# Kernel tuning notes

Hardware: AMD Instinct MI355X
Metric: run time of the kernel (lower is better)

Reference implementation:

```python
import jax, jax.numpy as jnp
import numpy as np

DIM = 256
HEADS = 8
HEAD_DIM = DIM // HEADS
B_, N = 8192, 49


def setup_inputs() -> dict:
    key = jax.random.key(0)
    k1, k2, k3, k4, k5, k6 = jax.random.split(key, 6)
    x = jax.random.normal(k1, (B_, N, DIM), dtype=jnp.float32)
    mask = jax.random.normal(k2, (B_, N, N), dtype=jnp.float32)
    s = 1.0 / np.sqrt(DIM)
    W_qkv = jax.random.normal(k3, (3 * DIM, DIM), dtype=jnp.float32) * s
    b_qkv = jax.random.normal(k4, (3 * DIM,), dtype=jnp.float32) * 0.02
    W_proj = jax.random.normal(k5, (DIM, DIM), dtype=jnp.float32) * s
    b_proj = jax.random.normal(k6, (DIM,), dtype=jnp.float32) * 0.02
    return {"x": x, "mask": mask, "W_qkv": W_qkv, "b_qkv": b_qkv,
            "W_proj": W_proj, "b_proj": b_proj}


def reference(x, mask, W_qkv, b_qkv, W_proj, b_proj):
    B, n, C = x.shape
    scale = HEAD_DIM ** (-0.5)
    # qkv projection: (B, N, 3C) -> (3, B, H, N, hd)
    qkv = x @ W_qkv.T + b_qkv
    qkv = qkv.reshape(B, n, 3, HEADS, HEAD_DIM).transpose(2, 0, 3, 1, 4)
    q, k, v = qkv[0], qkv[1], qkv[2]
    # scaled dot-product within each window
    attn = jnp.einsum('bhqd,bhkd->bhqk', q, k) * scale
    attn = attn + mask[:, None, :, :]  # additive window mask
    attn = jax.nn.softmax(attn, axis=-1)
    out = jnp.einsum('bhqk,bhkd->bhqd', attn, v)
    out = out.transpose(0, 2, 1, 3).reshape(B, n, C)
    return out @ W_proj.T + b_proj
```

## Files before the change

kernel.cpp:

```cpp
#include <hip/hip_runtime.h>
#include <hip/hip_bf16.h>

#define NTOK 49
#define DIMC 256

typedef __attribute__((ext_vector_type(8))) short bf16x8;
typedef __attribute__((ext_vector_type(4))) float f32x4;

__device__ __forceinline__ unsigned f2bf(float f) {
    union { float f; unsigned u; } v; v.f = f;
    return (v.u + 0x7FFFu + ((v.u >> 16) & 1u)) >> 16;
}

__global__ void convert_weights(const float* __restrict__ wq, const float* __restrict__ wp,
                                unsigned short* __restrict__ wqb, unsigned short* __restrict__ wpb) {
    int i = blockIdx.x * 256 + threadIdx.x;
    if (i < 768 * 256) wqb[i] = (unsigned short)f2bf(wq[i]);
    if (i < 256 * 256) wpb[i] = (unsigned short)f2bf(wp[i]);
}

__launch_bounds__(512, 2)
__global__ void win_attn_fused(const float* __restrict__ x, const float* __restrict__ mask,
                               const unsigned short* __restrict__ wqb, const float* __restrict__ bqkv,
                               const unsigned short* __restrict__ wpb, const float* __restrict__ bproj,
                               float* __restrict__ out) {
    __shared__ __align__(16) char lds[147456];
    char* const xb  = lds;
    char* const qb  = lds + 32768;
    char* const kb  = lds + 65536;
    char* const vtb = lds + 98304;
    char* const mb  = lds + 131072;

    const int b = blockIdx.x;
    const int tid = threadIdx.x;
    const int lane = tid & 63;
    const int wid = tid >> 6;
    const int c = lane & 15;
    const int g = lane >> 4;

    const f32x4 fzero = {0.f, 0.f, 0.f, 0.f};

    {
        const float* xw = x + (size_t)b * (NTOK * DIMC);
        #pragma unroll
        for (int it = 0; it < 8; ++it) {
            int idx = it * 512 + tid;
            int t = idx >> 6;
            int d0 = (idx & 63) * 4;
            float4 v = make_float4(0.f, 0.f, 0.f, 0.f);
            if (t < NTOK) v = *(const float4*)(xw + t * DIMC + d0);
            unsigned lo = f2bf(v.x) | (f2bf(v.y) << 16);
            unsigned hi = f2bf(v.z) | (f2bf(v.w) << 16);
            *(uint2*)(xb + t * 512 + ((d0 * 2) ^ ((t & 7) << 4))) = make_uint2(lo, hi);
        }
        const float* mw = mask + (size_t)b * (NTOK * NTOK);
        #pragma unroll
        for (int it = 0; it < 8; ++it) {
            int idx = it * 512 + tid;
            int q = idx >> 6;
            int key = idx & 63;
            float v;
            if (q < NTOK && key < NTOK) v = mw[q * NTOK + key];
            else v = (key >= NTOK) ? -1e30f : 0.f;
            *(float*)(mb + q * 256 + ((key * 4) ^ ((q & 7) << 4))) = v;
        }
    }
    __syncthreads();

    {
        f32x4 acc[6][4];
        #pragma unroll
        for (int j = 0; j < 6; ++j)
            #pragma unroll
            for (int mt = 0; mt < 4; ++mt)
                acc[j][mt] = fzero;

        #pragma unroll
        for (int ks = 0; ks < 8; ++ks) {
            const int kk = ks * 32 + g * 8;
            bf16x8 af[4];
            #pragma unroll
            for (int mt = 0; mt < 4; ++mt) {
                int t = mt * 16 + c;
                af[mt] = *(const bf16x8*)(xb + t * 512 + ((kk * 2) ^ ((t & 7) << 4)));
            }
            #pragma unroll
            for (int j = 0; j < 6; ++j) {
                int o = (wid + 8 * j) * 16 + c;
                bf16x8 bfr = *(const bf16x8*)(wqb + (size_t)o * 256 + kk);
                #pragma unroll
                for (int mt = 0; mt < 4; ++mt)
                    acc[j][mt] = __builtin_amdgcn_mfma_f32_16x16x32_bf16(af[mt], bfr, acc[j][mt], 0, 0, 0);
            }
        }

        #pragma unroll
        for (int j = 0; j < 6; ++j) {
            int nt = wid + 8 * j;
            int o = nt * 16 + c;
            float bias = bqkv[o];
            int sec = o >> 8;
            int oo = o & 255;
            int h = oo >> 5;
            int d = oo & 31;
            #pragma unroll
            for (int mt = 0; mt < 4; ++mt) {
                int t0 = mt * 16 + g * 4;
                f32x4 v = acc[j][mt];
                if (sec == 2) {
                    unsigned lo = f2bf(v[0] + bias) | (f2bf(v[1] + bias) << 16);
                    unsigned hi = f2bf(v[2] + bias) | (f2bf(v[3] + bias) << 16);
                    *(uint2*)(vtb + h * 4096 + d * 128 + ((t0 * 2) ^ ((d & 7) << 4))) = make_uint2(lo, hi);
                } else {
                    char* base = (sec == 0) ? qb : kb;
                    #pragma unroll
                    for (int r = 0; r < 4; ++r) {
                        int t = t0 + r;
                        *(unsigned short*)(base + h * 4096 + t * 64 + ((d * 2) ^ ((t & 3) << 4))) =
                            (unsigned short)f2bf(v[r] + bias);
                    }
                }
            }
        }
    }
    __syncthreads();

    f32x4 oacc[2][4];
    {
        const int h = wid;
        bf16x8 kf[4], qf[4];
        #pragma unroll
        for (int it = 0; it < 4; ++it) {
            int key = it * 16 + c;
            kf[it] = *(const bf16x8*)(kb + h * 4096 + key * 64 + ((g * 16) ^ ((key & 3) << 4)));
        }
        #pragma unroll
        for (int jt = 0; jt < 4; ++jt) {
            int q = jt * 16 + c;
            qf[jt] = *(const bf16x8*)(qb + h * 4096 + q * 64 + ((g * 16) ^ ((q & 3) << 4)));
        }
        float p[4][4][4];
        const float scale = 0.17677669529663687f;
        #pragma unroll
        for (int it = 0; it < 4; ++it) {
            #pragma unroll
            for (int jt = 0; jt < 4; ++jt) {
                f32x4 s = __builtin_amdgcn_mfma_f32_16x16x32_bf16(kf[it], qf[jt], fzero, 0, 0, 0);
                int q = jt * 16 + c;
                int key0 = it * 16 + g * 4;
                f32x4 mv = *(const f32x4*)(mb + q * 256 + ((key0 * 4) ^ ((q & 7) << 4)));
                #pragma unroll
                for (int r = 0; r < 4; ++r)
                    p[it][jt][r] = fmaf(s[r], scale, mv[r]);
            }
        }
        #pragma unroll
        for (int jt = 0; jt < 4; ++jt) {
            float m = -1e30f;
            #pragma unroll
            for (int it = 0; it < 4; ++it)
                #pragma unroll
                for (int r = 0; r < 4; ++r)
                    m = fmaxf(m, p[it][jt][r]);
            m = fmaxf(m, __shfl_xor(m, 16));
            m = fmaxf(m, __shfl_xor(m, 32));
            float ssum = 0.f;
            #pragma unroll
            for (int it = 0; it < 4; ++it)
                #pragma unroll
                for (int r = 0; r < 4; ++r) {
                    float e = __expf(p[it][jt][r] - m);
                    p[it][jt][r] = e;
                    ssum += e;
                }
            ssum += __shfl_xor(ssum, 16);
            ssum += __shfl_xor(ssum, 32);
            float inv = 1.0f / ssum;
            #pragma unroll
            for (int it = 0; it < 4; ++it)
                #pragma unroll
                for (int r = 0; r < 4; ++r)
                    p[it][jt][r] *= inv;
        }
        char* const pl = xb + wid * 4096;
        #pragma unroll
        for (int dt = 0; dt < 2; ++dt)
            #pragma unroll
            for (int jt = 0; jt < 4; ++jt)
                oacc[dt][jt] = fzero;

        #pragma unroll
        for (int kh = 0; kh < 2; ++kh) {
            #pragma unroll
            for (int it2 = 0; it2 < 2; ++it2) {
                int it = kh * 2 + it2;
                #pragma unroll
                for (int jt = 0; jt < 4; ++jt) {
                    int q = jt * 16 + c;
                    int keyh = it2 * 16 + g * 4;
                    unsigned lo = f2bf(p[it][jt][0]) | (f2bf(p[it][jt][1]) << 16);
                    unsigned hi = f2bf(p[it][jt][2]) | (f2bf(p[it][jt][3]) << 16);
                    *(uint2*)(pl + q * 64 + ((keyh * 2) ^ ((q & 3) << 4))) = make_uint2(lo, hi);
                }
            }
            bf16x8 vf[2];
            #pragma unroll
            for (int dt = 0; dt < 2; ++dt) {
                int d = dt * 16 + c;
                vf[dt] = *(const bf16x8*)(vtb + h * 4096 + d * 128 +
                                          (((kh * 32 + g * 8) * 2) ^ ((d & 7) << 4)));
            }
            #pragma unroll
            for (int jt = 0; jt < 4; ++jt) {
                int q = jt * 16 + c;
                bf16x8 pf = *(const bf16x8*)(pl + q * 64 + ((g * 16) ^ ((q & 3) << 4)));
                #pragma unroll
                for (int dt = 0; dt < 2; ++dt)
                    oacc[dt][jt] = __builtin_amdgcn_mfma_f32_16x16x32_bf16(vf[dt], pf, oacc[dt][jt], 0, 0, 0);
            }
        }
    }
    __syncthreads();

    {
        const int h = wid;
        #pragma unroll
        for (int dt = 0; dt < 2; ++dt) {
            #pragma unroll
            for (int jt = 0; jt < 4; ++jt) {
                int q = jt * 16 + c;
                int dg0 = h * 32 + dt * 16 + g * 4;
                f32x4 v = oacc[dt][jt];
                unsigned lo = f2bf(v[0]) | (f2bf(v[1]) << 16);
                unsigned hi = f2bf(v[2]) | (f2bf(v[3]) << 16);
                *(uint2*)(qb + q * 512 + ((dg0 * 2) ^ ((q & 7) << 4))) = make_uint2(lo, hi);
            }
        }
    }
    __syncthreads();

    {
        f32x4 pacc[2][4];
        #pragma unroll
        for (int j = 0; j < 2; ++j)
            #pragma unroll
            for (int mt = 0; mt < 4; ++mt)
                pacc[j][mt] = fzero;

        #pragma unroll
        for (int ks = 0; ks < 8; ++ks) {
            int kk = ks * 32 + g * 8;
            bf16x8 af[4];
            #pragma unroll
            for (int mt = 0; mt < 4; ++mt) {
                int t = mt * 16 + c;
                af[mt] = *(const bf16x8*)(qb + t * 512 + ((kk * 2) ^ ((t & 7) << 4)));
            }
            #pragma unroll
            for (int j = 0; j < 2; ++j) {
                int o = (wid * 2 + j) * 16 + c;
                bf16x8 bfr = *(const bf16x8*)(wpb + (size_t)o * 256 + kk);
                #pragma unroll
                for (int mt = 0; mt < 4; ++mt)
                    pacc[j][mt] = __builtin_amdgcn_mfma_f32_16x16x32_bf16(af[mt], bfr, pacc[j][mt], 0, 0, 0);
            }
        }
        float* ob = out + (size_t)b * (NTOK * DIMC);
        #pragma unroll
        for (int j = 0; j < 2; ++j) {
            int o = (wid * 2 + j) * 16 + c;
            float bias = bproj[o];
            #pragma unroll
            for (int mt = 0; mt < 4; ++mt) {
                #pragma unroll
                for (int r = 0; r < 4; ++r) {
                    int t = mt * 16 + g * 4 + r;
                    if (t < NTOK) ob[t * DIMC + o] = pacc[j][mt][r] + bias;
                }
            }
        }
    }
}

extern "C" void kernel_launch(void* const* d_in, const int* in_sizes, int n_in,
                              void* d_out, int out_size, void* d_ws, size_t ws_size,
                              hipStream_t stream) {
    const float* x    = (const float*)d_in[0];
    const float* mask = (const float*)d_in[1];
    const float* wq   = (const float*)d_in[2];
    const float* bq   = (const float*)d_in[3];
    const float* wp   = (const float*)d_in[4];
    const float* bp   = (const float*)d_in[5];
    float* o = (float*)d_out;

    unsigned short* wqb = (unsigned short*)d_ws;
    unsigned short* wpb = wqb + 768 * 256;

    convert_weights<<<768, 256, 0, stream>>>(wq, wp, wqb, wpb);
    win_attn_fused<<<8192, 512, 0, stream>>>(x, mask, wqb, bq, wpb, bp, o);
}
```

Measured before the change: 844.2 us.

## Keep per-head Q/K/V and probabilities in registers via shuffles, shrink LDS

Each wave now computes the Q, K and V projections for its own head directly, with the head-to-wave split reorganised so no cross-wave exchange is needed. Fragments are rearranged with lane shuffles instead of being staged through LDS, which also removes one block barrier and the LDS round trip for the softmax probabilities. LDS use drops from 144KB to 48KB and launch bounds rise to 4 blocks per CU, aiming for more occupancy and less LDS traffic. The attention scale is folded into Q before the bf16 rounding, and conversions now use the library bf16 intrinsic. In exchange there is more register pressure and shuffle overhead, and the x fragments are re-read from LDS for each of the three projections.

```diff
diff --git a/kernel.cpp b/kernel.cpp
--- a/kernel.cpp
+++ b/kernel.cpp
@@ -7,29 +7,48 @@
 typedef __attribute__((ext_vector_type(8))) short bf16x8;
 typedef __attribute__((ext_vector_type(4))) float f32x4;
 
-__device__ __forceinline__ unsigned f2bf(float f) {
-    union { float f; unsigned u; } v; v.f = f;
-    return (v.u + 0x7FFFu + ((v.u >> 16) & 1u)) >> 16;
+static __device__ __forceinline__ unsigned pk2(float a, float b) {
+    union { __hip_bfloat16 h; unsigned short u; } ua, ub;
+    ua.h = __float2bfloat16(a);
+    ub.h = __float2bfloat16(b);
+    return (unsigned)ua.u | ((unsigned)ub.u << 16);
+}
+
+static __device__ __forceinline__ bf16x8 mkfrag(unsigned w0, unsigned w1, unsigned w2, unsigned w3) {
+    union { bf16x8 v; unsigned u[4]; } t;
+    t.u[0] = w0; t.u[1] = w1; t.u[2] = w2; t.u[3] = w3;
+    return t.v;
+}
+
+static __device__ __forceinline__ unsigned sel2(unsigned lo, unsigned hi, int src, int ghi) {
+    unsigned a = __shfl(lo, src);
+    unsigned b = __shfl(hi, src);
+    return ghi ? b : a;
 }
 
 __global__ void convert_weights(const float* __restrict__ wq, const float* __restrict__ wp,
                                 unsigned short* __restrict__ wqb, unsigned short* __restrict__ wpb) {
     int i = blockIdx.x * 256 + threadIdx.x;
-    if (i < 768 * 256) wqb[i] = (unsigned short)f2bf(wq[i]);
-    if (i < 256 * 256) wpb[i] = (unsigned short)f2bf(wp[i]);
-}
-
-__launch_bounds__(512, 2)
+    if (i < 768 * 256) {
+        union { __hip_bfloat16 h; unsigned short u; } t;
+        t.h = __float2bfloat16(wq[i]);
+        wqb[i] = t.u;
+    }
+    if (i < 256 * 256) {
+        union { __hip_bfloat16 h; unsigned short u; } t;
+        t.h = __float2bfloat16(wp[i]);
+        wpb[i] = t.u;
+    }
+}
+
+__launch_bounds__(512, 4)
 __global__ void win_attn_fused(const float* __restrict__ x, const float* __restrict__ mask,
                                const unsigned short* __restrict__ wqb, const float* __restrict__ bqkv,
                                const unsigned short* __restrict__ wpb, const float* __restrict__ bproj,
                                float* __restrict__ out) {
-    __shared__ __align__(16) char lds[147456];
-    char* const xb  = lds;
-    char* const qb  = lds + 32768;
-    char* const kb  = lds + 65536;
-    char* const vtb = lds + 98304;
-    char* const mb  = lds + 131072;
+    __shared__ __align__(16) char lds[49152];
+    char* const xb = lds;
+    char* const mb = lds + 32768;
 
     const int b = blockIdx.x;
     const int tid = threadIdx.x;
@@ -49,9 +68,8 @@
             int d0 = (idx & 63) * 4;
             float4 v = make_float4(0.f, 0.f, 0.f, 0.f);
             if (t < NTOK) v = *(const float4*)(xw + t * DIMC + d0);
-            unsigned lo = f2bf(v.x) | (f2bf(v.y) << 16);
-            unsigned hi = f2bf(v.z) | (f2bf(v.w) << 16);
-            *(uint2*)(xb + t * 512 + ((d0 * 2) ^ ((t & 7) << 4))) = make_uint2(lo, hi);
+            *(uint2*)(xb + t * 512 + ((d0 * 2) ^ ((t & 7) << 4))) =
+                make_uint2(pk2(v.x, v.y), pk2(v.z, v.w));
         }
         const float* mw = mask + (size_t)b * (NTOK * NTOK);
         #pragma unroll
@@ -67,91 +85,111 @@
     }
     __syncthreads();
 
-    {
-        f32x4 acc[6][4];
-        #pragma unroll
-        for (int j = 0; j < 6; ++j)
-            #pragma unroll
-            for (int mt = 0; mt < 4; ++mt)
-                acc[j][mt] = fzero;
-
+    const int h = wid;
+    const int srcA = c + 16 * ((2 * g) & 3);
+    const int srcB = c + 16 * ((2 * g + 1) & 3);
+    const int ghi = g >> 1;
+    const float scale = 0.17677669529663687f;
+
+    #define XFRAG(t_, kk_) (*(const bf16x8*)(xb + (t_) * 512 + ((2 * ((kk_) + 8 * g)) ^ (((t_) & 7) << 4))))
+
+    unsigned kfw[4][4], qfw[4][4];
+    {
+        f32x4 acc[2][4];
+        #pragma unroll
+        for (int md = 0; md < 2; ++md)
+            #pragma unroll
+            for (int j2 = 0; j2 < 4; ++j2) acc[md][j2] = fzero;
         #pragma unroll
         for (int ks = 0; ks < 8; ++ks) {
-            const int kk = ks * 32 + g * 8;
-            bf16x8 af[4];
-            #pragma unroll
-            for (int mt = 0; mt < 4; ++mt) {
-                int t = mt * 16 + c;
-                af[mt] = *(const bf16x8*)(xb + t * 512 + ((kk * 2) ^ ((t & 7) << 4)));
-            }
-            #pragma unroll
-            for (int j = 0; j < 6; ++j) {
-                int o = (wid + 8 * j) * 16 + c;
-                bf16x8 bfr = *(const bf16x8*)(wqb + (size_t)o * 256 + kk);
-                #pragma unroll
-                for (int mt = 0; mt < 4; ++mt)
-                    acc[j][mt] = __builtin_amdgcn_mfma_f32_16x16x32_bf16(af[mt], bfr, acc[j][mt], 0, 0, 0);
-            }
-        }
-
-        #pragma unroll
-        for (int j = 0; j < 6; ++j) {
-            int nt = wid + 8 * j;
-            int o = nt * 16 + c;
-            float bias = bqkv[o];
-            int sec = o >> 8;
-            int oo = o & 255;
-            int h = oo >> 5;
-            int d = oo & 31;
-            #pragma unroll
-            for (int mt = 0; mt < 4; ++mt) {
-                int t0 = mt * 16 + g * 4;
-                f32x4 v = acc[j][mt];
-                if (sec == 2) {
-                    unsigned lo = f2bf(v[0] + bias) | (f2bf(v[1] + bias) << 16);
-                    unsigned hi = f2bf(v[2] + bias) | (f2bf(v[3] + bias) << 16);
-                    *(uint2*)(vtb + h * 4096 + d * 128 + ((t0 * 2) ^ ((d & 7) << 4))) = make_uint2(lo, hi);
-                } else {
-                    char* base = (sec == 0) ? qb : kb;
-                    #pragma unroll
-                    for (int r = 0; r < 4; ++r) {
-                        int t = t0 + r;
-                        *(unsigned short*)(base + h * 4096 + t * 64 + ((d * 2) ^ ((t & 3) << 4))) =
-                            (unsigned short)f2bf(v[r] + bias);
-                    }
-                }
-            }
-        }
-    }
-    __syncthreads();
-
-    f32x4 oacc[2][4];
-    {
-        const int h = wid;
-        bf16x8 kf[4], qf[4];
+            int kk = ks * 32;
+            bf16x8 bx[4];
+            #pragma unroll
+            for (int j2 = 0; j2 < 4; ++j2) { int t = j2 * 16 + c; bx[j2] = XFRAG(t, kk); }
+            #pragma unroll
+            for (int md = 0; md < 2; ++md) {
+                bf16x8 wa = *(const bf16x8*)(wqb + (256 + h * 32 + md * 16 + c) * 256 + kk + 8 * g);
+                #pragma unroll
+                for (int j2 = 0; j2 < 4; ++j2)
+                    acc[md][j2] = __builtin_amdgcn_mfma_f32_16x16x32_bf16(wa, bx[j2], acc[md][j2], 0, 0, 0);
+            }
+        }
+        unsigned kpp[2][4][2];
+        #pragma unroll
+        for (int md = 0; md < 2; ++md) {
+            const float* bk = bqkv + 256 + h * 32 + md * 16 + 4 * g;
+            float b0 = bk[0], b1 = bk[1], b2 = bk[2], b3 = bk[3];
+            #pragma unroll
+            for (int j2 = 0; j2 < 4; ++j2) {
+                kpp[md][j2][0] = pk2(acc[md][j2][0] + b0, acc[md][j2][1] + b1);
+                kpp[md][j2][1] = pk2(acc[md][j2][2] + b2, acc[md][j2][3] + b3);
+            }
+        }
         #pragma unroll
         for (int it = 0; it < 4; ++it) {
-            int key = it * 16 + c;
-            kf[it] = *(const bf16x8*)(kb + h * 4096 + key * 64 + ((g * 16) ^ ((key & 3) << 4)));
+            kfw[it][0] = sel2(kpp[0][it][0], kpp[1][it][0], srcA, ghi);
+            kfw[it][1] = sel2(kpp[0][it][1], kpp[1][it][1], srcA, ghi);
+            kfw[it][2] = sel2(kpp[0][it][0], kpp[1][it][0], srcB, ghi);
+            kfw[it][3] = sel2(kpp[0][it][1], kpp[1][it][1], srcB, ghi);
+        }
+    }
+
+    {
+        f32x4 acc[2][4];
+        #pragma unroll
+        for (int md = 0; md < 2; ++md)
+            #pragma unroll
+            for (int j2 = 0; j2 < 4; ++j2) acc[md][j2] = fzero;
+        #pragma unroll
+        for (int ks = 0; ks < 8; ++ks) {
+            int kk = ks * 32;
+            bf16x8 bx[4];
+            #pragma unroll
+            for (int j2 = 0; j2 < 4; ++j2) { int t = j2 * 16 + c; bx[j2] = XFRAG(t, kk); }
+            #pragma unroll
+            for (int md = 0; md < 2; ++md) {
+                bf16x8 wa = *(const bf16x8*)(wqb + (h * 32 + md * 16 + c) * 256 + kk + 8 * g);
+                #pragma unroll
+                for (int j2 = 0; j2 < 4; ++j2)
+                    acc[md][j2] = __builtin_amdgcn_mfma_f32_16x16x32_bf16(wa, bx[j2], acc[md][j2], 0, 0, 0);
+            }
+        }
+        unsigned qpp[2][4][2];
+        #pragma unroll
+        for (int md = 0; md < 2; ++md) {
+            const float* bq = bqkv + h * 32 + md * 16 + 4 * g;
+            float b0 = bq[0], b1 = bq[1], b2 = bq[2], b3 = bq[3];
+            #pragma unroll
+            for (int j2 = 0; j2 < 4; ++j2) {
+                qpp[md][j2][0] = pk2((acc[md][j2][0] + b0) * scale, (acc[md][j2][1] + b1) * scale);
+                qpp[md][j2][1] = pk2((acc[md][j2][2] + b2) * scale, (acc[md][j2][3] + b3) * scale);
+            }
         }
         #pragma unroll
         for (int jt = 0; jt < 4; ++jt) {
-            int q = jt * 16 + c;
-            qf[jt] = *(const bf16x8*)(qb + h * 4096 + q * 64 + ((g * 16) ^ ((q & 3) << 4)));
-        }
+            qfw[jt][0] = sel2(qpp[0][jt][0], qpp[1][jt][0], srcA, ghi);
+            qfw[jt][1] = sel2(qpp[0][jt][1], qpp[1][jt][1], srcA, ghi);
+            qfw[jt][2] = sel2(qpp[0][jt][0], qpp[1][jt][0], srcB, ghi);
+            qfw[jt][3] = sel2(qpp[0][jt][1], qpp[1][jt][1], srcB, ghi);
+        }
+    }
+
+    unsigned ppk[4][4][2];
+    {
         float p[4][4][4];
-        const float scale = 0.17677669529663687f;
         #pragma unroll
         for (int it = 0; it < 4; ++it) {
+            bf16x8 ka = mkfrag(kfw[it][0], kfw[it][1], kfw[it][2], kfw[it][3]);
             #pragma unroll
             for (int jt = 0; jt < 4; ++jt) {
-                f32x4 s = __builtin_amdgcn_mfma_f32_16x16x32_bf16(kf[it], qf[jt], fzero, 0, 0, 0);
+                bf16x8 qb_ = mkfrag(qfw[jt][0], qfw[jt][1], qfw[jt][2], qfw[jt][3]);
+                f32x4 s = __builtin_amdgcn_mfma_f32_16x16x32_bf16(ka, qb_, fzero, 0, 0, 0);
                 int q = jt * 16 + c;
                 int key0 = it * 16 + g * 4;
                 f32x4 mv = *(const f32x4*)(mb + q * 256 + ((key0 * 4) ^ ((q & 7) << 4)));
                 #pragma unroll
                 for (int r = 0; r < 4; ++r)
-                    p[it][jt][r] = fmaf(s[r], scale, mv[r]);
+                    p[it][jt][r] = s[r] + mv[r];
             }
         }
         #pragma unroll
@@ -182,59 +220,84 @@
                 for (int r = 0; r < 4; ++r)
                     p[it][jt][r] *= inv;
         }
-        char* const pl = xb + wid * 4096;
+        #pragma unroll
+        for (int it = 0; it < 4; ++it)
+            #pragma unroll
+            for (int jt = 0; jt < 4; ++jt) {
+                ppk[it][jt][0] = pk2(p[it][jt][0], p[it][jt][1]);
+                ppk[it][jt][1] = pk2(p[it][jt][2], p[it][jt][3]);
+            }
+    }
+
+    unsigned vpp[4][2][2];
+    {
+        f32x4 acc[4][2];
+        #pragma unroll
+        for (int mt = 0; mt < 4; ++mt)
+            #pragma unroll
+            for (int j2 = 0; j2 < 2; ++j2) acc[mt][j2] = fzero;
+        #pragma unroll
+        for (int ks = 0; ks < 8; ++ks) {
+            int kk = ks * 32;
+            bf16x8 ax[4];
+            #pragma unroll
+            for (int mt = 0; mt < 4; ++mt) { int t = mt * 16 + c; ax[mt] = XFRAG(t, kk); }
+            #pragma unroll
+            for (int j2 = 0; j2 < 2; ++j2) {
+                bf16x8 wb = *(const bf16x8*)(wqb + (512 + h * 32 + j2 * 16 + c) * 256 + kk + 8 * g);
+                #pragma unroll
+                for (int mt = 0; mt < 4; ++mt)
+                    acc[mt][j2] = __builtin_amdgcn_mfma_f32_16x16x32_bf16(ax[mt], wb, acc[mt][j2], 0, 0, 0);
+            }
+        }
+        float bv0 = bqkv[512 + h * 32 + c];
+        float bv1 = bqkv[512 + h * 32 + 16 + c];
+        #pragma unroll
+        for (int mt = 0; mt < 4; ++mt) {
+            vpp[mt][0][0] = pk2(acc[mt][0][0] + bv0, acc[mt][0][1] + bv0);
+            vpp[mt][0][1] = pk2(acc[mt][0][2] + bv0, acc[mt][0][3] + bv0);
+            vpp[mt][1][0] = pk2(acc[mt][1][0] + bv1, acc[mt][1][1] + bv1);
+            vpp[mt][1][1] = pk2(acc[mt][1][2] + bv1, acc[mt][1][3] + bv1);
+        }
+    }
+
+    f32x4 oacc[2][4];
+    #pragma unroll
+    for (int dt = 0; dt < 2; ++dt)
+        #pragma unroll
+        for (int jt = 0; jt < 4; ++jt) oacc[dt][jt] = fzero;
+    #pragma unroll
+    for (int kh = 0; kh < 2; ++kh) {
+        bf16x8 vf[2];
         #pragma unroll
         for (int dt = 0; dt < 2; ++dt)
-            #pragma unroll
-            for (int jt = 0; jt < 4; ++jt)
-                oacc[dt][jt] = fzero;
-
-        #pragma unroll
-        for (int kh = 0; kh < 2; ++kh) {
-            #pragma unroll
-            for (int it2 = 0; it2 < 2; ++it2) {
-                int it = kh * 2 + it2;
-                #pragma unroll
-                for (int jt = 0; jt < 4; ++jt) {
-                    int q = jt * 16 + c;
-                    int keyh = it2 * 16 + g * 4;
-                    unsigned lo = f2bf(p[it][jt][0]) | (f2bf(p[it][jt][1]) << 16);
-                    unsigned hi = f2bf(p[it][jt][2]) | (f2bf(p[it][jt][3]) << 16);
-                    *(uint2*)(pl + q * 64 + ((keyh * 2) ^ ((q & 3) << 4))) = make_uint2(lo, hi);
-                }
-            }
-            bf16x8 vf[2];
-            #pragma unroll
-            for (int dt = 0; dt < 2; ++dt) {
-                int d = dt * 16 + c;
-                vf[dt] = *(const bf16x8*)(vtb + h * 4096 + d * 128 +
-                                          (((kh * 32 + g * 8) * 2) ^ ((d & 7) << 4)));
-            }
-            #pragma unroll
-            for (int jt = 0; jt < 4; ++jt) {
-                int q = jt * 16 + c;
-                bf16x8 pf = *(const bf16x8*)(pl + q * 64 + ((g * 16) ^ ((q & 3) << 4)));
-                #pragma unroll
-                for (int dt = 0; dt < 2; ++dt)
-                    oacc[dt][jt] = __builtin_amdgcn_mfma_f32_16x16x32_bf16(vf[dt], pf, oacc[dt][jt], 0, 0, 0);
-            }
-        }
-    }
+            vf[dt] = mkfrag(sel2(vpp[2 * kh][dt][0], vpp[2 * kh + 1][dt][0], srcA, ghi),
+                            sel2(vpp[2 * kh][dt][1], vpp[2 * kh + 1][dt][1], srcA, ghi),
+                            sel2(vpp[2 * kh][dt][0], vpp[2 * kh + 1][dt][0], srcB, ghi),
+                            sel2(vpp[2 * kh][dt][1], vpp[2 * kh + 1][dt][1], srcB, ghi));
+        #pragma unroll
+        for (int jt = 0; jt < 4; ++jt) {
+            bf16x8 pf = mkfrag(sel2(ppk[2 * kh][jt][0], ppk[2 * kh + 1][jt][0], srcA, ghi),
+                               sel2(ppk[2 * kh][jt][1], ppk[2 * kh + 1][jt][1], srcA, ghi),
+                               sel2(ppk[2 * kh][jt][0], ppk[2 * kh + 1][jt][0], srcB, ghi),
+                               sel2(ppk[2 * kh][jt][1], ppk[2 * kh + 1][jt][1], srcB, ghi));
+            #pragma unroll
+            for (int dt = 0; dt < 2; ++dt)
+                oacc[dt][jt] = __builtin_amdgcn_mfma_f32_16x16x32_bf16(vf[dt], pf, oacc[dt][jt], 0, 0, 0);
+        }
+    }
+
     __syncthreads();
 
-    {
-        const int h = wid;
-        #pragma unroll
-        for (int dt = 0; dt < 2; ++dt) {
-            #pragma unroll
-            for (int jt = 0; jt < 4; ++jt) {
-                int q = jt * 16 + c;
-                int dg0 = h * 32 + dt * 16 + g * 4;
-                f32x4 v = oacc[dt][jt];
-                unsigned lo = f2bf(v[0]) | (f2bf(v[1]) << 16);
-                unsigned hi = f2bf(v[2]) | (f2bf(v[3]) << 16);
-                *(uint2*)(qb + q * 512 + ((dg0 * 2) ^ ((q & 7) << 4))) = make_uint2(lo, hi);
-            }
+    #pragma unroll
+    for (int dt = 0; dt < 2; ++dt) {
+        #pragma unroll
+        for (int jt = 0; jt < 4; ++jt) {
+            int q = jt * 16 + c;
+            int d0 = h * 32 + dt * 16 + 4 * g;
+            f32x4 v = oacc[dt][jt];
+            *(uint2*)(xb + q * 512 + ((2 * d0) ^ ((q & 7) << 4))) =
+                make_uint2(pk2(v[0], v[1]), pk2(v[2], v[3]));
         }
     }
     __syncthreads();
@@ -244,22 +307,18 @@
         #pragma unroll
         for (int j = 0; j < 2; ++j)
             #pragma unroll
-            for (int mt = 0; mt < 4; ++mt)
-                pacc[j][mt] = fzero;
+            for (int mt = 0; mt < 4; ++mt) pacc[j][mt] = fzero;
 
         #pragma unroll
         for (int ks = 0; ks < 8; ++ks) {
-            int kk = ks * 32 + g * 8;
+            int kk = ks * 32;
             bf16x8 af[4];
             #pragma unroll
-            for (int mt = 0; mt < 4; ++mt) {
-                int t = mt * 16 + c;
-                af[mt] = *(const bf16x8*)(qb + t * 512 + ((kk * 2) ^ ((t & 7) << 4)));
-            }
+            for (int mt = 0; mt < 4; ++mt) { int t = mt * 16 + c; af[mt] = XFRAG(t, kk); }
             #pragma unroll
             for (int j = 0; j < 2; ++j) {
                 int o = (wid * 2 + j) * 16 + c;
-                bf16x8 bfr = *(const bf16x8*)(wpb + (size_t)o * 256 + kk);
+                bf16x8 bfr = *(const bf16x8*)(wpb + (size_t)o * 256 + kk + 8 * g);
                 #pragma unroll
                 for (int mt = 0; mt < 4; ++mt)
                     pacc[j][mt] = __builtin_amdgcn_mfma_f32_16x16x32_bf16(af[mt], bfr, pacc[j][mt], 0, 0, 0);
@@ -280,6 +339,7 @@
             }
         }
     }
+    #undef XFRAG
 }
 
 extern "C" void kernel_launch(void* const* d_in, const int* in_sizes, int n_in,
```

After: 1.513 ms. 1.79x slower.
